# Performance work log

Hardware: AMD Instinct MI355X
Metric: run time of the kernel (lower is better)

The kernel has to match this reference:

```python
import jax, jax.numpy as jnp
import numpy as np

BN_EPS = 1e-3  # Keras BatchNormalization default epsilon
K = 7          # kernel_size


def setup_inputs() -> dict:
    key = jax.random.key(0)
    ks = jax.random.split(key, 5)
    B, L, C, F = 128, 512, 128, 128
    L_out = L - K + 1  # 506, valid padding, stride 1
    x = jax.random.normal(ks[0], (B, L, C), dtype=jnp.float32)
    # LocallyConnected1D unshared weights: (L_out, K*C, F), lecun_normal ~ N(0, 1/fan_in)
    kernel = jax.random.normal(ks[1], (L_out, K * C, F), dtype=jnp.float32) * (1.0 / np.sqrt(K * C))
    bias = jnp.zeros((L_out, F), dtype=jnp.float32)
    gamma = jnp.ones((F,), dtype=jnp.float32)
    beta = jnp.zeros((F,), dtype=jnp.float32)
    moving_mean = jax.random.normal(ks[2], (F,), dtype=jnp.float32) * 0.1
    moving_var = jax.random.uniform(ks[3], (F,), dtype=jnp.float32, minval=0.5, maxval=1.5)
    return {"x": x, "kernel": kernel, "bias": bias, "gamma": gamma,
            "beta": beta, "moving_mean": moving_mean, "moving_var": moving_var}


def _local_block(x, kernel, bias, gamma, beta, moving_mean, moving_var):
    B, L, C = x.shape
    L_out = L - K + 1
    F = kernel.shape[-1]
    # Patch extraction: idx[l, k] = l + k -> patches (B, L_out, K, C)
    idx = jnp.arange(L_out)[:, None] + jnp.arange(K)[None, :]
    patches = x[:, idx, :]                                  # (B, L_out, K, C)
    w = kernel.reshape(L_out, K, C, F)                      # unshared per-position weights
    y = jnp.einsum('blkc,lkcf->blf', patches, w) + bias     # (B, L_out, F)
    # BatchNorm (inference, axis=-1) fused with affine
    inv = gamma * jax.lax.rsqrt(moving_var + BN_EPS)
    y = y * inv + (beta - moving_mean * inv)
    return jax.nn.relu(y)


def reference(x, kernel, bias, gamma, beta, moving_mean, moving_var):
    return _local_block(x, kernel, bias, gamma, beta, moving_mean, moving_var)
```

## Files before the change

### kernel.cpp

```cpp
#include <hip/hip_runtime.h>

#define LO 506
#define LL 512
#define CC 128
#define FF 128
#define KC 896
#define BK 32
#define NK 28
#define XS 40
#define WS 40

typedef __attribute__((ext_vector_type(8))) short short8;
typedef __attribute__((ext_vector_type(4))) float floatx4;
typedef __attribute__((ext_vector_type(4))) unsigned int uintx4;
typedef unsigned short ushort_t;

static __device__ __forceinline__ ushort_t f2bf(float f) {
    union { float f; unsigned int u; } c; c.f = f;
    unsigned int u = c.u;
    return (ushort_t)((u + 0x7fffu + ((u >> 16) & 1u)) >> 16);
}
static __device__ __forceinline__ unsigned int pk2(float a, float b) {
    return (unsigned int)f2bf(a) | ((unsigned int)f2bf(b) << 16);
}

__global__ __launch_bounds__(512, 4)
void local_block_kernel(const float* __restrict__ x,
                        const float* __restrict__ wg,
                        const float* __restrict__ bias,
                        const float* __restrict__ gamma,
                        const float* __restrict__ beta,
                        const float* __restrict__ mmean,
                        const float* __restrict__ mvar,
                        float* __restrict__ out)
{
    const int bid = blockIdx.x;
    const int xcd = bid & 7;
    const int idx = bid >> 3;
    const int q8  = LO >> 3;
    const int r8  = LO & 7;
    const int l   = (xcd < r8) ? xcd * (q8 + 1) + idx
                               : r8 * (q8 + 1) + (xcd - r8) * q8 + idx;

    const int t    = threadIdx.x;
    const int lane = t & 63;
    const int wave = t >> 6;
    const int q    = lane >> 4;
    const int l16  = lane & 15;
    const int wr   = wave >> 1;
    const int wc   = wave & 1;

    __shared__ __align__(16) ushort_t Xs[2][128 * XS];
    __shared__ __align__(16) ushort_t Wt[2][128 * WS];

    const int am  = t >> 2;
    const int ak0 = (t & 3) * 8;
    const float* aptr = x + (size_t)am * (LL * CC) + l * CC + ak0;

    const int wf  = t & 127;
    const int wk  = (t >> 7) * 8;
    const float* wptr = wg + (size_t)l * (KC * FF) + wf;

    floatx4 acc[2][4] = {};

    floatx4 areg0[2], areg1[2];
    float   wreg0[8], wreg1[8];

#define LOAD_A(AR, KT) { const float* p = aptr + (KT) * BK;                     \
        AR[0] = *(const floatx4*)(p);                                           \
        AR[1] = *(const floatx4*)(p + 4); }

#define LOAD_W(WR, KT) { const float* p = wptr + (size_t)((KT) * BK + wk) * FF; \
        _Pragma("unroll") for (int j = 0; j < 8; ++j)                           \
            WR[j] = __builtin_nontemporal_load(p + j * FF); }

#define STAGE(S, AR, WR) {                                                      \
        uintx4 av = { pk2(AR[0].x, AR[0].y), pk2(AR[0].z, AR[0].w),             \
                      pk2(AR[1].x, AR[1].y), pk2(AR[1].z, AR[1].w) };           \
        *(uintx4*)&Xs[S][am * XS + ak0] = av;                                   \
        uintx4 wv = { pk2(WR[0], WR[1]), pk2(WR[2], WR[3]),                     \
                      pk2(WR[4], WR[5]), pk2(WR[6], WR[7]) };                   \
        *(uintx4*)&Wt[S][wf * WS + wk] = wv; }

#define BAR() {                                                                 \
        asm volatile("s_waitcnt lgkmcnt(0)" ::: "memory");                      \
        __builtin_amdgcn_s_barrier();                                           \
        asm volatile("" ::: "memory"); }

#define COMPUTE(S) {                                                            \
        short8 af[2], bfr[4];                                                   \
        _Pragma("unroll") for (int mi = 0; mi < 2; ++mi)                        \
            af[mi] = *(const short8*)&Xs[S][(wr*32 + mi*16 + l16) * XS + q*8];  \
        _Pragma("unroll") for (int ni = 0; ni < 4; ++ni)                        \
            bfr[ni] = *(const short8*)&Wt[S][(wc*64 + ni*16 + l16) * WS + q*8]; \
        _Pragma("unroll") for (int mi = 0; mi < 2; ++mi)                        \
            _Pragma("unroll") for (int ni = 0; ni < 4; ++ni)                    \
                acc[mi][ni] = __builtin_amdgcn_mfma_f32_16x16x32_bf16(          \
                    af[mi], bfr[ni], acc[mi][ni], 0, 0, 0); }

    LOAD_A(areg0, 0); LOAD_W(wreg0, 0);
    LOAD_A(areg1, 1); LOAD_W(wreg1, 1);

    for (int kt = 0; kt < NK; kt += 2) {
        STAGE(0, areg0, wreg0);
        if (kt + 2 < NK) { LOAD_A(areg0, kt + 2); LOAD_W(wreg0, kt + 2); }
        BAR();
        COMPUTE(0);
        STAGE(1, areg1, wreg1);
        if (kt + 3 < NK) { LOAD_A(areg1, kt + 3); LOAD_W(wreg1, kt + 3); }
        BAR();
        COMPUTE(1);
    }

#pragma unroll
    for (int ni = 0; ni < 4; ++ni) {
        int f = wc*64 + ni*16 + l16;
        float inv = gamma[f] * rsqrtf(mvar[f] + 1e-3f);
        float off = bias[l * FF + f] * inv + beta[f] - mmean[f] * inv;
#pragma unroll
        for (int mi = 0; mi < 2; ++mi) {
#pragma unroll
            for (int rg = 0; rg < 4; ++rg) {
                int b = wr*32 + mi*16 + q*4 + rg;
                float v = acc[mi][ni][rg] * inv + off;
                __builtin_nontemporal_store(fmaxf(v, 0.0f),
                    &out[((size_t)b * LO + l) * FF + f]);
            }
        }
    }
#undef LOAD_A
#undef LOAD_W
#undef STAGE
#undef BAR
#undef COMPUTE
}

extern "C" void kernel_launch(void* const* d_in, const int* in_sizes, int n_in,
                              void* d_out, int out_size, void* d_ws, size_t ws_size,
                              hipStream_t stream) {
    const float* x     = (const float*)d_in[0];
    const float* w     = (const float*)d_in[1];
    const float* bias  = (const float*)d_in[2];
    const float* gamma = (const float*)d_in[3];
    const float* beta  = (const float*)d_in[4];
    const float* mmean = (const float*)d_in[5];
    const float* mvar  = (const float*)d_in[6];
    float* out = (float*)d_out;

    local_block_kernel<<<dim3(LO), dim3(512), 0, stream>>>(
        x, w, bias, gamma, beta, mmean, mvar, out);
}
```

Measured before the change: 347.2 us.

## Process two adjacent output positions per block to reuse input tiles

Each block now computes two neighbouring output positions, loading the shared sliding input window once and applying each position's weights to its overlapping k-range. This roughly halves redundant input loads and bf16 conversions from global memory. In exchange, the grid shrinks to 253 blocks, register use grows with two accumulator sets and the occupancy hint drops, which may reduce latency hiding.

```diff
diff --git a/kernel.cpp b/kernel.cpp
--- a/kernel.cpp
+++ b/kernel.cpp
@@ -6,7 +6,10 @@
 #define FF 128
 #define KC 896
 #define BK 32
-#define NK 28
+#define NT 32
+#define G0 28
+#define G1 4
+#define NB 253
 #define XS 40
 #define WS 40
 
@@ -24,7 +27,7 @@
     return (unsigned int)f2bf(a) | ((unsigned int)f2bf(b) << 16);
 }
 
-__global__ __launch_bounds__(512, 4)
+__global__ __launch_bounds__(512, 2)
 void local_block_kernel(const float* __restrict__ x,
                         const float* __restrict__ wg,
                         const float* __restrict__ bias,
@@ -37,10 +40,12 @@
     const int bid = blockIdx.x;
     const int xcd = bid & 7;
     const int idx = bid >> 3;
-    const int q8  = LO >> 3;
-    const int r8  = LO & 7;
-    const int l   = (xcd < r8) ? xcd * (q8 + 1) + idx
+    const int q8  = NB >> 3;
+    const int r8  = NB & 7;
+    const int g   = (xcd < r8) ? xcd * (q8 + 1) + idx
                                : r8 * (q8 + 1) + (xcd - r8) * q8 + idx;
+    const int l0  = g * 2;
+    const int l1  = l0 + 1;
 
     const int t    = threadIdx.x;
     const int lane = t & 63;
@@ -50,89 +55,124 @@
     const int wr   = wave >> 1;
     const int wc   = wave & 1;
 
-    __shared__ __align__(16) ushort_t Xs[2][128 * XS];
-    __shared__ __align__(16) ushort_t Wt[2][128 * WS];
+    __shared__ __align__(16) ushort_t Xs [2][128 * XS];
+    __shared__ __align__(16) ushort_t W0s[2][128 * WS];
+    __shared__ __align__(16) ushort_t W1s[2][128 * WS];
 
     const int am  = t >> 2;
     const int ak0 = (t & 3) * 8;
-    const float* aptr = x + (size_t)am * (LL * CC) + l * CC + ak0;
+    const float* aptr = x + (size_t)am * (LL * CC) + l0 * CC + ak0;
 
     const int wf  = t & 127;
     const int wk  = (t >> 7) * 8;
-    const float* wptr = wg + (size_t)l * (KC * FF) + wf;
+    const float* wptr0 = wg + (size_t)l0 * (KC * FF) + wf;
+    const float* wptr1 = wg + (size_t)l1 * (KC * FF) + wf;
 
-    floatx4 acc[2][4] = {};
+    floatx4 acc0[2][4] = {};
+    floatx4 acc1[2][4] = {};
 
-    floatx4 areg0[2], areg1[2];
-    float   wreg0[8], wreg1[8];
+    floatx4 arg0[2], arg1[2];
+    float   w0r0[8], w0r1[8];
+    float   w1r0[8], w1r1[8];
 
 #define LOAD_A(AR, KT) { const float* p = aptr + (KT) * BK;                     \
         AR[0] = *(const floatx4*)(p);                                           \
         AR[1] = *(const floatx4*)(p + 4); }
 
-#define LOAD_W(WR, KT) { const float* p = wptr + (size_t)((KT) * BK + wk) * FF; \
+#define LOAD_W(WR, PTR, KOFF) { const float* p = (PTR) + (size_t)((KOFF) + wk) * FF; \
         _Pragma("unroll") for (int j = 0; j < 8; ++j)                           \
             WR[j] = __builtin_nontemporal_load(p + j * FF); }
 
-#define STAGE(S, AR, WR) {                                                      \
+#define STAGE_A(S, AR) {                                                        \
         uintx4 av = { pk2(AR[0].x, AR[0].y), pk2(AR[0].z, AR[0].w),             \
                       pk2(AR[1].x, AR[1].y), pk2(AR[1].z, AR[1].w) };           \
-        *(uintx4*)&Xs[S][am * XS + ak0] = av;                                   \
+        *(uintx4*)&Xs[S][am * XS + ak0] = av; }
+
+#define STAGE_W(S, DST, WR) {                                                   \
         uintx4 wv = { pk2(WR[0], WR[1]), pk2(WR[2], WR[3]),                     \
                       pk2(WR[4], WR[5]), pk2(WR[6], WR[7]) };                   \
-        *(uintx4*)&Wt[S][wf * WS + wk] = wv; }
+        *(uintx4*)&DST[S][wf * WS + wk] = wv; }
 
 #define BAR() {                                                                 \
         asm volatile("s_waitcnt lgkmcnt(0)" ::: "memory");                      \
         __builtin_amdgcn_s_barrier();                                           \
         asm volatile("" ::: "memory"); }
 
-#define COMPUTE(S) {                                                            \
-        short8 af[2], bfr[4];                                                   \
-        _Pragma("unroll") for (int mi = 0; mi < 2; ++mi)                        \
-            af[mi] = *(const short8*)&Xs[S][(wr*32 + mi*16 + l16) * XS + q*8];  \
+#define GEMM(S, SRC, ACC, AF) {                                                 \
+        short8 bfr[4];                                                          \
         _Pragma("unroll") for (int ni = 0; ni < 4; ++ni)                        \
-            bfr[ni] = *(const short8*)&Wt[S][(wc*64 + ni*16 + l16) * WS + q*8]; \
+            bfr[ni] = *(const short8*)&SRC[S][(wc*64 + ni*16 + l16) * WS + q*8];\
         _Pragma("unroll") for (int mi = 0; mi < 2; ++mi)                        \
             _Pragma("unroll") for (int ni = 0; ni < 4; ++ni)                    \
-                acc[mi][ni] = __builtin_amdgcn_mfma_f32_16x16x32_bf16(          \
-                    af[mi], bfr[ni], acc[mi][ni], 0, 0, 0); }
+                ACC[mi][ni] = __builtin_amdgcn_mfma_f32_16x16x32_bf16(          \
+                    AF[mi], bfr[ni], ACC[mi][ni], 0, 0, 0); }
 
-    LOAD_A(areg0, 0); LOAD_W(wreg0, 0);
-    LOAD_A(areg1, 1); LOAD_W(wreg1, 1);
+#define LOAD_AF(S, AF) {                                                        \
+        _Pragma("unroll") for (int mi = 0; mi < 2; ++mi)                        \
+            AF[mi] = *(const short8*)&Xs[S][(wr*32 + mi*16 + l16) * XS + q*8]; }
 
-    for (int kt = 0; kt < NK; kt += 2) {
-        STAGE(0, areg0, wreg0);
-        if (kt + 2 < NK) { LOAD_A(areg0, kt + 2); LOAD_W(wreg0, kt + 2); }
+    LOAD_A(arg0, 0); LOAD_W(w0r0, wptr0, 0 * BK);
+    LOAD_A(arg1, 1); LOAD_W(w0r1, wptr0, 1 * BK);
+
+    for (int kt = 0; kt < NT; kt += 2) {
+        const bool p0 = (kt < G0);
+        const bool p1 = (kt >= G1);
+
+        STAGE_A(0, arg0);
+        if (p0) STAGE_W(0, W0s, w0r0);
+        if (p1) STAGE_W(0, W1s, w1r0);
+        if (kt + 2 < NT) LOAD_A(arg0, kt + 2);
+        if (kt + 2 < G0) LOAD_W(w0r0, wptr0, (kt + 2) * BK);
+        if (kt + 2 >= G1) LOAD_W(w1r0, wptr1, (kt + 2) * BK - 128);
         BAR();
-        COMPUTE(0);
-        STAGE(1, areg1, wreg1);
-        if (kt + 3 < NK) { LOAD_A(areg1, kt + 3); LOAD_W(wreg1, kt + 3); }
+        {
+            short8 af[2]; LOAD_AF(0, af);
+            if (p0) GEMM(0, W0s, acc0, af);
+            if (p1) GEMM(0, W1s, acc1, af);
+        }
+
+        STAGE_A(1, arg1);
+        if (p0) STAGE_W(1, W0s, w0r1);
+        if (p1) STAGE_W(1, W1s, w1r1);
+        if (kt + 3 < NT) LOAD_A(arg1, kt + 3);
+        if (kt + 3 < G0) LOAD_W(w0r1, wptr0, (kt + 3) * BK);
+        if (kt + 3 >= G1) LOAD_W(w1r1, wptr1, (kt + 3) * BK - 128);
         BAR();
-        COMPUTE(1);
+        {
+            short8 af[2]; LOAD_AF(1, af);
+            if (p0) GEMM(1, W0s, acc0, af);
+            if (p1) GEMM(1, W1s, acc1, af);
+        }
     }
 
 #pragma unroll
     for (int ni = 0; ni < 4; ++ni) {
         int f = wc*64 + ni*16 + l16;
-        float inv = gamma[f] * rsqrtf(mvar[f] + 1e-3f);
-        float off = bias[l * FF + f] * inv + beta[f] - mmean[f] * inv;
+        float inv  = gamma[f] * rsqrtf(mvar[f] + 1e-3f);
+        float bcom = beta[f] - mmean[f] * inv;
+        float off0 = bias[l0 * FF + f] * inv + bcom;
+        float off1 = bias[l1 * FF + f] * inv + bcom;
 #pragma unroll
         for (int mi = 0; mi < 2; ++mi) {
 #pragma unroll
             for (int rg = 0; rg < 4; ++rg) {
                 int b = wr*32 + mi*16 + q*4 + rg;
-                float v = acc[mi][ni][rg] * inv + off;
-                __builtin_nontemporal_store(fmaxf(v, 0.0f),
-                    &out[((size_t)b * LO + l) * FF + f]);
+                float v0 = acc0[mi][ni][rg] * inv + off0;
+                float v1 = acc1[mi][ni][rg] * inv + off1;
+                __builtin_nontemporal_store(fmaxf(v0, 0.0f),
+                    &out[((size_t)b * LO + l0) * FF + f]);
+                __builtin_nontemporal_store(fmaxf(v1, 0.0f),
+                    &out[((size_t)b * LO + l1) * FF + f]);
             }
         }
     }
 #undef LOAD_A
 #undef LOAD_W
-#undef STAGE
+#undef STAGE_A
+#undef STAGE_W
 #undef BAR
-#undef COMPUTE
+#undef GEMM
+#undef LOAD_AF
 }
 
 extern "C" void kernel_launch(void* const* d_in, const int* in_sizes, int n_in,
@@ -147,6 +187,6 @@
     const float* mvar  = (const float*)d_in[6];
     float* out = (float*)d_out;
 
-    local_block_kernel<<<dim3(LO), dim3(512), 0, stream>>>(
+    local_block_kernel<<<dim3(NB), dim3(512), 0, stream>>>(
         x, w, bias, gamma, beta, mmean, mvar, out);
 }
```

After: 348.4 us. About the same (+0.3%).
